# Performance work log

Measured on AMD Instinct MI355X. Metric: run time of the kernel, lower is better.

The kernel has to match this reference:

```python
import jax, jax.numpy as jnp
import numpy as np

N = 100000   # nodes
E = 1600000  # edges (before self-loops)
IN = 128     # in_dim
H = 32       # hidden (hardcoded in module)
G = 2048     # graphs in batch
NEG_SLOPE = 0.2  # PyG GATConv default leaky_relu slope


def setup_inputs() -> dict:
    key = jax.random.key(0)
    ks = jax.random.split(key, 20)
    inp = {
        "x": jax.random.normal(ks[0], (N, IN), jnp.float32),
        "edge_index": jax.random.randint(ks[1], (2, E), 0, N, dtype=jnp.int64),
        "batch": jnp.sort(jax.random.randint(ks[2], (N,), 0, G, dtype=jnp.int64)),
    }
    dims = [(IN, H), (H, H), (H, H), (H, H)]
    for i, (di, do) in enumerate(dims, start=1):
        k = 3 + 4 * (i - 1)
        inp[f"W{i}"] = jax.random.normal(ks[k], (di, do), jnp.float32) * 0.1
        inp[f"a_s{i}"] = jax.random.normal(ks[k + 1], (do,), jnp.float32) * 0.1
        inp[f"a_d{i}"] = jax.random.normal(ks[k + 2], (do,), jnp.float32) * 0.1
        inp[f"b{i}"] = jnp.zeros((do,), jnp.float32)
    return inp


def _gat(x, src, dst, W, a_s, a_d, b):
    # PyG GATConv, heads=1: h = xW; e_ij = leaky_relu(a_s.h_j + a_d.h_i);
    # alpha = softmax over incoming edges of i; out_i = sum_j alpha_ij * h_j + b
    h = x @ W                                # [N, H]
    es = h @ a_s                             # [N]
    ed = h @ a_d                             # [N]
    e = jax.nn.leaky_relu(es[src] + ed[dst], NEG_SLOPE)   # [E+N]
    m = jax.ops.segment_max(e, dst, num_segments=N)        # per-dest max (stable softmax)
    ex = jnp.exp(e - m[dst])
    denom = jax.ops.segment_sum(ex, dst, num_segments=N)
    alpha = ex / denom[dst]
    out = jax.ops.segment_sum(alpha[:, None] * h[src], dst, num_segments=N)
    return out + b


def reference(x, edge_index, batch, W1, a_s1, a_d1, b1, W2, a_s2, a_d2, b2,
              W3, a_s3, a_d3, b3, W4, a_s4, a_d4, b4):
    # add self-loops once (GATConv add_self_loops=True; same edge set every layer)
    loop = jnp.arange(N, dtype=edge_index.dtype)
    src = jnp.concatenate([edge_index[0], loop])
    dst = jnp.concatenate([edge_index[1], loop])
    x = _gat(x, src, dst, W1, a_s1, a_d1, b1)  # tanh in source is a no-op (result discarded)
    x = _gat(x, src, dst, W2, a_s2, a_d2, b2)
    x = _gat(x, src, dst, W3, a_s3, a_d3, b3)
    x = _gat(x, src, dst, W4, a_s4, a_d4, b4)
    # global_mean_pool
    sums = jax.ops.segment_sum(x, batch, num_segments=G)
    cnt = jax.ops.segment_sum(jnp.ones((N,), x.dtype), batch, num_segments=G)
    return sums / jnp.maximum(cnt, 1.0)[:, None]
```

## Files before the change

kernel.cpp:

```cpp
#include <hip/hip_runtime.h>
#include <hip/hip_fp16.h>

#define HDIM 32
#define IN_DIM 128
#define NEG_SLOPE 0.2f
#define NPB 128
#define NPB_SHIFT 7
#define MAXB 1024
#define CHUNK 8192
#define CAP 4096

typedef _Float16 half8  __attribute__((ext_vector_type(8)));
typedef _Float16 half4v __attribute__((ext_vector_type(4)));
typedef float    floatx4 __attribute__((ext_vector_type(4)));

__device__ __forceinline__ float leaky(float e) {
    return (e >= 0.f) ? e : NEG_SLOPE * e;
}

__device__ __forceinline__ float2 h2f(unsigned int u) {
    __half2 h = *reinterpret_cast<__half2*>(&u);
    return __half22float2(h);
}


template<int K>
__global__ __launch_bounds__(256) void gemm_mfma(
    const float* __restrict__ x, const float* __restrict__ W,
    const float* __restrict__ a_s, const float* __restrict__ a_d,
    __half* __restrict__ h, float* __restrict__ es, float* __restrict__ ed, int N)
{
    constexpr int KP = K + 8;
    __shared__ _Float16 xs[64 * KP];
    __shared__ _Float16 Wt[32 * KP];
    const int tid = threadIdx.x;
    for (int i = tid; i < K * 32; i += 256) {
        int k = i >> 5, n = i & 31;
        Wt[n * KP + k] = (_Float16)W[i];
    }
    const int lane = tid & 63;
    const int wave = tid >> 6;
    const int m16  = lane & 15;
    const int quad = lane >> 4;
    const float as0 = a_s[m16], as1 = a_s[m16 + 16];
    const float ad0 = a_d[m16], ad1 = a_d[m16 + 16];

    const int ntiles = (N + 63) >> 6;
    for (int tile = blockIdx.x; tile < ntiles; tile += gridDim.x) {
        const int row0 = tile << 6;
        __syncthreads();
        for (int i = tid; i < 64 * (K / 4); i += 256) {
            int r  = i / (K / 4);
            int c4 = i % (K / 4);
            float4 v = (row0 + r < N) ? ((const float4*)x)[(size_t)(row0 + r) * (K / 4) + c4]
                                      : make_float4(0.f, 0.f, 0.f, 0.f);
            half4v hv = { (_Float16)v.x, (_Float16)v.y, (_Float16)v.z, (_Float16)v.w };
            *(half4v*)&xs[r * KP + c4 * 4] = hv;
        }
        __syncthreads();
        floatx4 acc0 = {0.f, 0.f, 0.f, 0.f}, acc1 = {0.f, 0.f, 0.f, 0.f};
        const int rbase = wave * 16;
        #pragma unroll
        for (int kt = 0; kt < K / 32; kt++) {
            half8 a  = *(half8*)&xs[(rbase + m16) * KP + kt * 32 + quad * 8];
            half8 b0 = *(half8*)&Wt[m16 * KP + kt * 32 + quad * 8];
            half8 b1 = *(half8*)&Wt[(m16 + 16) * KP + kt * 32 + quad * 8];
            acc0 = __builtin_amdgcn_mfma_f32_16x16x32_f16(a, b0, acc0, 0, 0, 0);
            acc1 = __builtin_amdgcn_mfma_f32_16x16x32_f16(a, b1, acc1, 0, 0, 0);
        }
        #pragma unroll
        for (int r = 0; r < 4; r++) {
            int row = row0 + rbase + quad * 4 + r;
            float c0 = acc0[r], c1 = acc1[r];
            float ps = c0 * as0 + c1 * as1;
            float pd = c0 * ad0 + c1 * ad1;
            #pragma unroll
            for (int m = 8; m >= 1; m >>= 1) { ps += __shfl_xor(ps, m); pd += __shfl_xor(pd, m); }
            if (row < N) {
                h[(size_t)row * HDIM + m16]      = __float2half(c0);
                h[(size_t)row * HDIM + m16 + 16] = __float2half(c1);
                if (m16 == 0) { es[row] = ps; ed[row] = pd; }
            }
        }
    }
}


__global__ __launch_bounds__(256) void chunk_hist(
    const int* __restrict__ dsts, int E, int B, int* __restrict__ cnt2D)
{
    __shared__ int hist[MAXB];
    const int blk = blockIdx.x;
    for (int i = threadIdx.x; i < B; i += 256) hist[i] = 0;
    __syncthreads();
    const int e0 = blk * CHUNK;
    for (int i = threadIdx.x; i < CHUNK; i += 256) {
        int e = e0 + i;
        if (e < E) atomicAdd(&hist[dsts[e] >> NPB_SHIFT], 1);
    }
    __syncthreads();
    for (int i = threadIdx.x; i < B; i += 256) cnt2D[(size_t)blk * B + i] = hist[i];
}

__global__ __launch_bounds__(256) void chunk_scan(
    const int* __restrict__ cnt2D, int NBLK, int B,
    int* __restrict__ off2D, int* __restrict__ bcnt)
{
    __shared__ int s[256];
    const int b = blockIdx.x, t = threadIdx.x;
    int v = (t < NBLK) ? cnt2D[(size_t)t * B + b] : 0;
    s[t] = v;
    __syncthreads();
    for (int off = 1; off < 256; off <<= 1) {
        int add = (t >= off) ? s[t - off] : 0;
        __syncthreads();
        s[t] += add;
        __syncthreads();
    }
    if (t < NBLK) off2D[(size_t)t * B + b] = s[t] - v;
    if (t == 255) bcnt[b] = s[255];
}

__global__ __launch_bounds__(1024) void bucket_scan(
    const int* __restrict__ bcnt, int B, int E,
    int* __restrict__ bstart, int* __restrict__ rowptr, int N)
{
    __shared__ int s[1024];
    const int t = threadIdx.x;
    int v = (t < B) ? bcnt[t] : 0;
    s[t] = v;
    __syncthreads();
    for (int off = 1; off < 1024; off <<= 1) {
        int add = (t >= off) ? s[t - off] : 0;
        __syncthreads();
        s[t] += add;
        __syncthreads();
    }
    if (t < B) bstart[t] = s[t] - v;
    if (t == 0) { bstart[B] = E; rowptr[N] = E; }
}

__global__ __launch_bounds__(256) void pair_scatter2(
    const int* __restrict__ srcs, const int* __restrict__ dsts, int E, int B,
    const int* __restrict__ off2D, const int* __restrict__ bstart,
    int* __restrict__ pairs)
{
    __shared__ int cur[MAXB];
    const int blk = blockIdx.x;
    for (int i = threadIdx.x; i < B; i += 256)
        cur[i] = bstart[i] + off2D[(size_t)blk * B + i];
    __syncthreads();
    const int e0 = blk * CHUNK;
    for (int i = threadIdx.x; i < CHUNK; i += 256) {
        int e = e0 + i;
        if (e < E) {
            int s = srcs[e], d = dsts[e];
            int pos = atomicAdd(&cur[d >> NPB_SHIFT], 1);
            pairs[pos] = (s << NPB_SHIFT) | (d & (NPB - 1));
        }
    }
}

__global__ __launch_bounds__(256) void bucket_sort(
    const int* __restrict__ pairs, const int* __restrict__ bstart,
    int* __restrict__ rowptr, int* __restrict__ csrsrc, int N)
{
    __shared__ int ldeg[NPB];
    __shared__ int lex[NPB];
    __shared__ int recs[CAP];
    __shared__ int sorted[CAP];
    const int b = blockIdx.x, t = threadIdx.x;
    const int p0 = bstart[b], p1 = bstart[b + 1];
    const int cnt = p1 - p0;
    if (t < NPB) ldeg[t] = 0;
    __syncthreads();
    for (int i = t; i < cnt; i += 256) {
        int r = pairs[p0 + i];
        atomicAdd(&ldeg[r & (NPB - 1)], 1);
        if (i < CAP) recs[i] = r;
    }
    __syncthreads();
    if (t < NPB) lex[t] = ldeg[t];
    __syncthreads();
    for (int off = 1; off < NPB; off <<= 1) {
        int add = (t >= off && t < NPB) ? lex[t - off] : 0;
        __syncthreads();
        if (t < NPB) lex[t] += add;
        __syncthreads();
    }
    const int node0 = b * NPB;
    if (t < NPB) {
        int excl = lex[t] - ldeg[t];
        if (node0 + t < N) rowptr[node0 + t] = p0 + excl;
        ldeg[t] = excl;
    }
    __syncthreads();
    if (cnt <= CAP) {
        for (int i = t; i < cnt; i += 256) {
            int r = recs[i];
            int pos = atomicAdd(&ldeg[r & (NPB - 1)], 1);
            sorted[pos] = r >> NPB_SHIFT;
        }
        __syncthreads();
        for (int i = t; i < cnt; i += 256) csrsrc[p0 + i] = sorted[i];
    } else {
        for (int i = t; i < cnt; i += 256) {
            int r = pairs[p0 + i];
            int pos = atomicAdd(&ldeg[r & (NPB - 1)], 1);
            csrsrc[p0 + pos] = r >> NPB_SHIFT;
        }
    }
}


__global__ __launch_bounds__(256) void agg5(
    const __half* __restrict__ h, const float* __restrict__ es, const float* __restrict__ ed,
    const int* __restrict__ rowptr, const int* __restrict__ csrsrc,
    const float* __restrict__ a_s, const float* __restrict__ b,
    float* __restrict__ out, int N)
{
    const int gid  = blockIdx.x * 256 + threadIdx.x;
    const int node = gid >> 2;
    const int l    = threadIdx.x & 3;
    if (node >= N) return;

    const int e0 = rowptr[node];
    const int e1 = rowptr[node + 1];
    const float edi = ed[node];
    const uint4* __restrict__ h16 = (const uint4*)h;

    float asf[8];
    #pragma unroll
    for (int i = 0; i < 8; i++) asf[i] = a_s[l * 8 + i];

    float a0=0.f,a1=0.f,a2=0.f,a3=0.f,a4=0.f,a5=0.f,a6=0.f,a7=0.f,den=0.f;

    int e = e0;
    for (; e + 8 <= e1; e += 8) {
        int s[8]; uint4 u[8];
        #pragma unroll
        for (int j = 0; j < 8; j++) s[j] = csrsrc[e + j];
        #pragma unroll
        for (int j = 0; j < 8; j++) u[j] = h16[(size_t)s[j] * 4 + l];
        #pragma unroll
        for (int j = 0; j < 8; j++) {
            float2 f0 = h2f(u[j].x), f1 = h2f(u[j].y), f2 = h2f(u[j].z), f3 = h2f(u[j].w);
            float dot = asf[0]*f0.x + asf[1]*f0.y + asf[2]*f1.x + asf[3]*f1.y
                      + asf[4]*f2.x + asf[5]*f2.y + asf[6]*f3.x + asf[7]*f3.y;
            dot += __shfl_xor(dot, 1);
            dot += __shfl_xor(dot, 2);
            float w = __expf(leaky(dot + edi));
            den += w;
            a0 += w*f0.x; a1 += w*f0.y; a2 += w*f1.x; a3 += w*f1.y;
            a4 += w*f2.x; a5 += w*f2.y; a6 += w*f3.x; a7 += w*f3.y;
        }
    }
    for (; e < e1; e++) {
        int s = csrsrc[e];
        uint4 u = h16[(size_t)s * 4 + l];
        float2 f0 = h2f(u.x), f1 = h2f(u.y), f2 = h2f(u.z), f3 = h2f(u.w);
        float dot = asf[0]*f0.x + asf[1]*f0.y + asf[2]*f1.x + asf[3]*f1.y
                  + asf[4]*f2.x + asf[5]*f2.y + asf[6]*f3.x + asf[7]*f3.y;
        dot += __shfl_xor(dot, 1);
        dot += __shfl_xor(dot, 2);
        float w = __expf(leaky(dot + edi));
        den += w;
        a0 += w*f0.x; a1 += w*f0.y; a2 += w*f1.x; a3 += w*f1.y;
        a4 += w*f2.x; a5 += w*f2.y; a6 += w*f3.x; a7 += w*f3.y;
    }
    {
        float wt = __expf(leaky(es[node] + edi));
        uint4 u = h16[(size_t)node * 4 + l];
        float2 f0 = h2f(u.x), f1 = h2f(u.y), f2 = h2f(u.z), f3 = h2f(u.w);
        den += wt;
        a0 += wt*f0.x; a1 += wt*f0.y; a2 += wt*f1.x; a3 += wt*f1.y;
        a4 += wt*f2.x; a5 += wt*f2.y; a6 += wt*f3.x; a7 += wt*f3.y;
    }
    const float4* b4 = (const float4*)b;
    float4 bv0 = b4[2*l], bv1 = b4[2*l + 1];
    float inv = 1.f / den;
    float4 o0, o1;
    o0.x = a0*inv + bv0.x; o0.y = a1*inv + bv0.y; o0.z = a2*inv + bv0.z; o0.w = a3*inv + bv0.w;
    o1.x = a4*inv + bv1.x; o1.y = a5*inv + bv1.y; o1.z = a6*inv + bv1.z; o1.w = a7*inv + bv1.w;
    ((float4*)out)[(size_t)node*8 + 2*l]     = o0;
    ((float4*)out)[(size_t)node*8 + 2*l + 1] = o1;
}


__global__ __launch_bounds__(256) void pool_graph(
    const float* __restrict__ x, const int* __restrict__ batch,
    float* __restrict__ out, int N, int G)
{
    const int g = (blockIdx.x * 256 + threadIdx.x) >> 6;
    if (g >= G) return;
    const int lane = threadIdx.x & 63;
    const int feat = lane & 31;
    const int half = lane >> 5;

    int lo = 0, hi = N;
    while (lo < hi) { int mid = (lo + hi) >> 1; if (batch[mid] < g) lo = mid + 1; else hi = mid; }
    const int start = lo;
    int lo2 = start, hi2 = N;
    while (lo2 < hi2) { int mid = (lo2 + hi2) >> 1; if (batch[mid] < g + 1) lo2 = mid + 1; else hi2 = mid; }
    const int end = lo2;

    float acc = 0.f;
    for (int i = start + half; i < end; i += 2)
        acc += x[(size_t)i * HDIM + feat];
    acc += __shfl_xor(acc, 32);
    if (half == 0) {
        float cnt = (float)(end - start);
        out[(size_t)g * HDIM + feat] = acc / fmaxf(cnt, 1.f);
    }
}


extern "C" void kernel_launch(void* const* d_in, const int* in_sizes, int n_in,
                              void* d_out, int out_size, void* d_ws, size_t ws_size,
                              hipStream_t stream) {
    const float* x          = (const float*)d_in[0];
    const int*   edge_index = (const int*)d_in[1];
    const int*   batch      = (const int*)d_in[2];

    const int N = in_sizes[2];
    const int E = in_sizes[1] / 2;
    const int G = out_size / HDIM;
    const int B = (N + NPB - 1) / NPB;
    const int NBLK = (E + CHUNK - 1) / CHUNK;
    const int ntiles = (N + 63) / 64;

    const int* srcs = edge_index;
    const int* dsts = edge_index + E;

    char* p = (char*)d_ws;
    __half* h     = (__half*)p; p += (size_t)N * HDIM * sizeof(__half);
    float* xbuf   = (float*)p; p += (size_t)N * HDIM * sizeof(float);
    float* es     = (float*)p; p += (size_t)N * sizeof(float);
    float* ed     = (float*)p; p += (size_t)N * sizeof(float);
    int*   rowptr = (int*)p;   p += (size_t)(N + 1) * sizeof(int);
    int*   csrsrc = (int*)p;   p += (size_t)E * sizeof(int);
    int*   pairs  = (int*)p;   p += (size_t)E * sizeof(int);
    int*   cnt2D  = (int*)p;   p += (size_t)NBLK * B * sizeof(int);
    int*   off2D  = (int*)p;   p += (size_t)NBLK * B * sizeof(int);
    int*   bcnt   = (int*)p;   p += (size_t)B * sizeof(int);
    int*   bstart = (int*)p;   p += (size_t)(B + 1) * sizeof(int);

    chunk_hist  <<<NBLK, 256, 0, stream>>>(dsts, E, B, cnt2D);
    chunk_scan  <<<B, 256, 0, stream>>>(cnt2D, NBLK, B, off2D, bcnt);
    bucket_scan <<<1, 1024, 0, stream>>>(bcnt, B, E, bstart, rowptr, N);
    pair_scatter2<<<NBLK, 256, 0, stream>>>(srcs, dsts, E, B, off2D, bstart, pairs);
    bucket_sort <<<B, 256, 0, stream>>>(pairs, bstart, rowptr, csrsrc, N);

    for (int l = 0; l < 4; l++) {
        const float* W   = (const float*)d_in[3 + 4 * l];
        const float* a_s = (const float*)d_in[4 + 4 * l];
        const float* a_d = (const float*)d_in[5 + 4 * l];
        const float* bb  = (const float*)d_in[6 + 4 * l];

        if (l == 0) gemm_mfma<IN_DIM><<<ntiles, 256, 0, stream>>>(x, W, a_s, a_d, h, es, ed, N);
        else        gemm_mfma<HDIM>  <<<ntiles, 256, 0, stream>>>(xbuf, W, a_s, a_d, h, es, ed, N);

        agg5<<<(N * 4 + 255) / 256, 256, 0, stream>>>(h, es, ed, rowptr, csrsrc, a_s, bb, xbuf, N);
    }

    pool_graph<<<(G * 64 + 255) / 256, 256, 0, stream>>>(xbuf, batch, (float*)d_out, N, G);
}
```

Measured before the change: 346.5 us.

## Fuse next-layer 32x32 projection into aggregation and compute attention scores on the fly

The aggregation kernel now multiplies each node's output by the next layer's 32x32 weight matrix held in shared memory and writes fp16 h directly. This removes three separate gemm launches and the fp32 xbuf round trip between layers. The per-node es/ed scores are no longer produced by the gemm; they are recomputed from the node's own h row inside aggregation. This adds per-thread register pressure (a 32-float row plus a 32-step FMA loop) and an LDS weight load per block, which may reduce occupancy of the gather-bound kernel.

```diff
diff --git a/kernel.cpp b/kernel.cpp
--- a/kernel.cpp
+++ b/kernel.cpp
@@ -27,8 +27,7 @@
 template<int K>
 __global__ __launch_bounds__(256) void gemm_mfma(
     const float* __restrict__ x, const float* __restrict__ W,
-    const float* __restrict__ a_s, const float* __restrict__ a_d,
-    __half* __restrict__ h, float* __restrict__ es, float* __restrict__ ed, int N)
+    __half* __restrict__ h, int N)
 {
     constexpr int KP = K + 8;
     __shared__ _Float16 xs[64 * KP];
@@ -42,8 +41,6 @@
     const int wave = tid >> 6;
     const int m16  = lane & 15;
     const int quad = lane >> 4;
-    const float as0 = a_s[m16], as1 = a_s[m16 + 16];
-    const float ad0 = a_d[m16], ad1 = a_d[m16 + 16];
 
     const int ntiles = (N + 63) >> 6;
     for (int tile = blockIdx.x; tile < ntiles; tile += gridDim.x) {
@@ -71,15 +68,9 @@
         #pragma unroll
         for (int r = 0; r < 4; r++) {
             int row = row0 + rbase + quad * 4 + r;
-            float c0 = acc0[r], c1 = acc1[r];
-            float ps = c0 * as0 + c1 * as1;
-            float pd = c0 * ad0 + c1 * ad1;
-            #pragma unroll
-            for (int m = 8; m >= 1; m >>= 1) { ps += __shfl_xor(ps, m); pd += __shfl_xor(pd, m); }
             if (row < N) {
-                h[(size_t)row * HDIM + m16]      = __float2half(c0);
-                h[(size_t)row * HDIM + m16 + 16] = __float2half(c1);
-                if (m16 == 0) { es[row] = ps; ed[row] = pd; }
+                h[(size_t)row * HDIM + m16]      = __float2half(acc0[r]);
+                h[(size_t)row * HDIM + m16 + 16] = __float2half(acc1[r]);
             }
         }
     }
@@ -213,12 +204,20 @@
 }
 
 
-__global__ __launch_bounds__(256) void agg5(
-    const __half* __restrict__ h, const float* __restrict__ es, const float* __restrict__ ed,
+template<bool LAST>
+__global__ __launch_bounds__(256) void agg_fused(
+    const __half* __restrict__ h,
     const int* __restrict__ rowptr, const int* __restrict__ csrsrc,
-    const float* __restrict__ a_s, const float* __restrict__ b,
-    float* __restrict__ out, int N)
-{
+    const float* __restrict__ a_s, const float* __restrict__ a_d,
+    const float* __restrict__ b, const float* __restrict__ Wn,
+    __half* __restrict__ hn, float* __restrict__ outbuf, int N)
+{
+    __shared__ float Ws[HDIM * HDIM];
+    if (!LAST) {
+        for (int i = threadIdx.x; i < HDIM * HDIM; i += 256) Ws[i] = Wn[i];
+        __syncthreads();
+    }
+
     const int gid  = blockIdx.x * 256 + threadIdx.x;
     const int node = gid >> 2;
     const int l    = threadIdx.x & 3;
@@ -226,12 +225,21 @@
 
     const int e0 = rowptr[node];
     const int e1 = rowptr[node + 1];
-    const float edi = ed[node];
     const uint4* __restrict__ h16 = (const uint4*)h;
 
-    float asf[8];
+    float asf[8], adf[8];
     #pragma unroll
-    for (int i = 0; i < 8; i++) asf[i] = a_s[l * 8 + i];
+    for (int i = 0; i < 8; i++) { asf[i] = a_s[l * 8 + i]; adf[i] = a_d[l * 8 + i]; }
+
+    uint4 uself = h16[(size_t)node * 4 + l];
+    float2 g0 = h2f(uself.x), g1 = h2f(uself.y), g2 = h2f(uself.z), g3 = h2f(uself.w);
+    float dsl = asf[0]*g0.x + asf[1]*g0.y + asf[2]*g1.x + asf[3]*g1.y
+              + asf[4]*g2.x + asf[5]*g2.y + asf[6]*g3.x + asf[7]*g3.y;
+    float ddl = adf[0]*g0.x + adf[1]*g0.y + adf[2]*g1.x + adf[3]*g1.y
+              + adf[4]*g2.x + adf[5]*g2.y + adf[6]*g3.x + adf[7]*g3.y;
+    dsl += __shfl_xor(dsl, 1); dsl += __shfl_xor(dsl, 2);
+    ddl += __shfl_xor(ddl, 1); ddl += __shfl_xor(ddl, 2);
+    const float edi = ddl;
 
     float a0=0.f,a1=0.f,a2=0.f,a3=0.f,a4=0.f,a5=0.f,a6=0.f,a7=0.f,den=0.f;
 
@@ -269,21 +277,44 @@
         a4 += w*f2.x; a5 += w*f2.y; a6 += w*f3.x; a7 += w*f3.y;
     }
     {
-        float wt = __expf(leaky(es[node] + edi));
-        uint4 u = h16[(size_t)node * 4 + l];
-        float2 f0 = h2f(u.x), f1 = h2f(u.y), f2 = h2f(u.z), f3 = h2f(u.w);
-        den += wt;
-        a0 += wt*f0.x; a1 += wt*f0.y; a2 += wt*f1.x; a3 += wt*f1.y;
-        a4 += wt*f2.x; a5 += wt*f2.y; a6 += wt*f3.x; a7 += wt*f3.y;
-    }
+        float w = __expf(leaky(dsl + edi));
+        den += w;
+        a0 += w*g0.x; a1 += w*g0.y; a2 += w*g1.x; a3 += w*g1.y;
+        a4 += w*g2.x; a5 += w*g2.y; a6 += w*g3.x; a7 += w*g3.y;
+    }
+
     const float4* b4 = (const float4*)b;
     float4 bv0 = b4[2*l], bv1 = b4[2*l + 1];
     float inv = 1.f / den;
-    float4 o0, o1;
-    o0.x = a0*inv + bv0.x; o0.y = a1*inv + bv0.y; o0.z = a2*inv + bv0.z; o0.w = a3*inv + bv0.w;
-    o1.x = a4*inv + bv1.x; o1.y = a5*inv + bv1.y; o1.z = a6*inv + bv1.z; o1.w = a7*inv + bv1.w;
-    ((float4*)out)[(size_t)node*8 + 2*l]     = o0;
-    ((float4*)out)[(size_t)node*8 + 2*l + 1] = o1;
+    float o[8];
+    o[0] = a0*inv + bv0.x; o[1] = a1*inv + bv0.y; o[2] = a2*inv + bv0.z; o[3] = a3*inv + bv0.w;
+    o[4] = a4*inv + bv1.x; o[5] = a5*inv + bv1.y; o[6] = a6*inv + bv1.z; o[7] = a7*inv + bv1.w;
+
+    if (LAST) {
+        float4 o0 = { o[0], o[1], o[2], o[3] };
+        float4 o1 = { o[4], o[5], o[6], o[7] };
+        ((float4*)outbuf)[(size_t)node*8 + 2*l]     = o0;
+        ((float4*)outbuf)[(size_t)node*8 + 2*l + 1] = o1;
+    } else {
+        float row[32];
+        #pragma unroll
+        for (int bb = 0; bb < 4; bb++) {
+            #pragma unroll
+            for (int j = 0; j < 8; j++) row[bb*8 + j] = __shfl(o[j], bb, 4);
+        }
+        float hn8[8] = {0.f,0.f,0.f,0.f,0.f,0.f,0.f,0.f};
+        #pragma unroll
+        for (int k = 0; k < 32; k++) {
+            float4 wa = *(const float4*)&Ws[k*32 + l*8];
+            float4 wb = *(const float4*)&Ws[k*32 + l*8 + 4];
+            float rk = row[k];
+            hn8[0] += rk*wa.x; hn8[1] += rk*wa.y; hn8[2] += rk*wa.z; hn8[3] += rk*wa.w;
+            hn8[4] += rk*wb.x; hn8[5] += rk*wb.y; hn8[6] += rk*wb.z; hn8[7] += rk*wb.w;
+        }
+        half8 v = { (_Float16)hn8[0], (_Float16)hn8[1], (_Float16)hn8[2], (_Float16)hn8[3],
+                    (_Float16)hn8[4], (_Float16)hn8[5], (_Float16)hn8[6], (_Float16)hn8[7] };
+        *(half8*)((_Float16*)hn + (size_t)node*32 + l*8) = v;
+    }
 }
 
 
@@ -333,11 +364,11 @@
     const int* dsts = edge_index + E;
 
     char* p = (char*)d_ws;
-    __half* h     = (__half*)p; p += (size_t)N * HDIM * sizeof(__half);
+    __half* h_a   = (__half*)p; p += (size_t)N * HDIM * sizeof(__half);
+    __half* h_b   = (__half*)p; p += (size_t)N * HDIM * sizeof(__half);
     float* xbuf   = (float*)p; p += (size_t)N * HDIM * sizeof(float);
-    float* es     = (float*)p; p += (size_t)N * sizeof(float);
-    float* ed     = (float*)p; p += (size_t)N * sizeof(float);
     int*   rowptr = (int*)p;   p += (size_t)(N + 1) * sizeof(int);
+    p += 16 - ((size_t)p & 15);
     int*   csrsrc = (int*)p;   p += (size_t)E * sizeof(int);
     int*   pairs  = (int*)p;   p += (size_t)E * sizeof(int);
     int*   cnt2D  = (int*)p;   p += (size_t)NBLK * B * sizeof(int);
@@ -351,17 +382,30 @@
     pair_scatter2<<<NBLK, 256, 0, stream>>>(srcs, dsts, E, B, off2D, bstart, pairs);
     bucket_sort <<<B, 256, 0, stream>>>(pairs, bstart, rowptr, csrsrc, N);
 
-    for (int l = 0; l < 4; l++) {
-        const float* W   = (const float*)d_in[3 + 4 * l];
-        const float* a_s = (const float*)d_in[4 + 4 * l];
-        const float* a_d = (const float*)d_in[5 + 4 * l];
-        const float* bb  = (const float*)d_in[6 + 4 * l];
-
-        if (l == 0) gemm_mfma<IN_DIM><<<ntiles, 256, 0, stream>>>(x, W, a_s, a_d, h, es, ed, N);
-        else        gemm_mfma<HDIM>  <<<ntiles, 256, 0, stream>>>(xbuf, W, a_s, a_d, h, es, ed, N);
-
-        agg5<<<(N * 4 + 255) / 256, 256, 0, stream>>>(h, es, ed, rowptr, csrsrc, a_s, bb, xbuf, N);
-    }
+    const float* W1   = (const float*)d_in[3];
+    const float* as1  = (const float*)d_in[4];
+    const float* ad1  = (const float*)d_in[5];
+    const float* b1   = (const float*)d_in[6];
+    const float* W2   = (const float*)d_in[7];
+    const float* as2  = (const float*)d_in[8];
+    const float* ad2  = (const float*)d_in[9];
+    const float* b2   = (const float*)d_in[10];
+    const float* W3   = (const float*)d_in[11];
+    const float* as3  = (const float*)d_in[12];
+    const float* ad3  = (const float*)d_in[13];
+    const float* b3   = (const float*)d_in[14];
+    const float* W4   = (const float*)d_in[15];
+    const float* as4  = (const float*)d_in[16];
+    const float* ad4  = (const float*)d_in[17];
+    const float* b4   = (const float*)d_in[18];
+
+    const int aggGrid = (N * 4 + 255) / 256;
+
+    gemm_mfma<IN_DIM><<<ntiles, 256, 0, stream>>>(x, W1, h_a, N);
+    agg_fused<false><<<aggGrid, 256, 0, stream>>>(h_a, rowptr, csrsrc, as1, ad1, b1, W2, h_b, xbuf, N);
+    agg_fused<false><<<aggGrid, 256, 0, stream>>>(h_b, rowptr, csrsrc, as2, ad2, b2, W3, h_a, xbuf, N);
+    agg_fused<false><<<aggGrid, 256, 0, stream>>>(h_a, rowptr, csrsrc, as3, ad3, b3, W4, h_b, xbuf, N);
+    agg_fused<true> <<<aggGrid, 256, 0, stream>>>(h_b, rowptr, csrsrc, as4, ad4, b4, W4, h_a, xbuf, N);
 
     pool_graph<<<(G * 64 + 255) / 256, 256, 0, stream>>>(xbuf, batch, (float*)d_out, N, G);
 }
```

Result: slower. 363.8 us (+5.0%).

## Sort nodes by degree for aggregation and compute self attention scores in-kernel

Applied to the files above, without the earlier changes.

Adds a degree-bucketed permutation of destination nodes (histogram, scan and scatter kernels run once), so that aggregation waves process nodes with similar in-degree and suffer less divergence. It also removes the es/ed outputs from the GEMM epilogue and recomputes the self node's source and destination scores inside the aggregation kernel from the self row it already loads. The cost is three extra setup kernels, an indirect perm lookup, and output writes scattered across nodes instead of sequential, which can hurt coalescing and locality.

```diff
diff --git a/kernel.cpp b/kernel.cpp
--- a/kernel.cpp
+++ b/kernel.cpp
@@ -9,6 +9,7 @@
 #define MAXB 1024
 #define CHUNK 8192
 #define CAP 4096
+#define DBINS 128
 
 typedef _Float16 half8  __attribute__((ext_vector_type(8)));
 typedef _Float16 half4v __attribute__((ext_vector_type(4)));
@@ -27,8 +28,7 @@
 template<int K>
 __global__ __launch_bounds__(256) void gemm_mfma(
     const float* __restrict__ x, const float* __restrict__ W,
-    const float* __restrict__ a_s, const float* __restrict__ a_d,
-    __half* __restrict__ h, float* __restrict__ es, float* __restrict__ ed, int N)
+    __half* __restrict__ h, int N)
 {
     constexpr int KP = K + 8;
     __shared__ _Float16 xs[64 * KP];
@@ -42,8 +42,6 @@
     const int wave = tid >> 6;
     const int m16  = lane & 15;
     const int quad = lane >> 4;
-    const float as0 = a_s[m16], as1 = a_s[m16 + 16];
-    const float ad0 = a_d[m16], ad1 = a_d[m16 + 16];
 
     const int ntiles = (N + 63) >> 6;
     for (int tile = blockIdx.x; tile < ntiles; tile += gridDim.x) {
@@ -71,15 +69,9 @@
         #pragma unroll
         for (int r = 0; r < 4; r++) {
             int row = row0 + rbase + quad * 4 + r;
-            float c0 = acc0[r], c1 = acc1[r];
-            float ps = c0 * as0 + c1 * as1;
-            float pd = c0 * ad0 + c1 * ad1;
-            #pragma unroll
-            for (int m = 8; m >= 1; m >>= 1) { ps += __shfl_xor(ps, m); pd += __shfl_xor(pd, m); }
             if (row < N) {
-                h[(size_t)row * HDIM + m16]      = __float2half(c0);
-                h[(size_t)row * HDIM + m16 + 16] = __float2half(c1);
-                if (m16 == 0) { es[row] = ps; ed[row] = pd; }
+                h[(size_t)row * HDIM + m16]      = __float2half(acc0[r]);
+                h[(size_t)row * HDIM + m16 + 16] = __float2half(acc1[r]);
             }
         }
     }
@@ -213,25 +205,78 @@
 }
 
 
-__global__ __launch_bounds__(256) void agg5(
-    const __half* __restrict__ h, const float* __restrict__ es, const float* __restrict__ ed,
+__global__ __launch_bounds__(256) void deg_hist(
+    const int* __restrict__ rowptr, int N, int* __restrict__ dhist)
+{
+    int i = blockIdx.x * 256 + threadIdx.x;
+    if (i < N) {
+        int d = rowptr[i + 1] - rowptr[i];
+        if (d > DBINS - 1) d = DBINS - 1;
+        atomicAdd(&dhist[d], 1);
+    }
+}
+
+__global__ __launch_bounds__(DBINS) void deg_scan(
+    const int* __restrict__ dhist, int* __restrict__ dcur)
+{
+    __shared__ int s[DBINS];
+    int t = threadIdx.x;
+    int v = dhist[t];
+    s[t] = v;
+    __syncthreads();
+    for (int off = 1; off < DBINS; off <<= 1) {
+        int add = (t >= off) ? s[t - off] : 0;
+        __syncthreads();
+        s[t] += add;
+        __syncthreads();
+    }
+    dcur[t] = s[t] - v;
+}
+
+__global__ __launch_bounds__(256) void deg_scatter(
+    const int* __restrict__ rowptr, int N,
+    int* __restrict__ dcur, int* __restrict__ perm)
+{
+    int i = blockIdx.x * 256 + threadIdx.x;
+    if (i < N) {
+        int d = rowptr[i + 1] - rowptr[i];
+        if (d > DBINS - 1) d = DBINS - 1;
+        int pos = atomicAdd(&dcur[d], 1);
+        perm[pos] = i;
+    }
+}
+
+
+__global__ __launch_bounds__(256) void agg6(
+    const __half* __restrict__ h,
     const int* __restrict__ rowptr, const int* __restrict__ csrsrc,
-    const float* __restrict__ a_s, const float* __restrict__ b,
-    float* __restrict__ out, int N)
-{
-    const int gid  = blockIdx.x * 256 + threadIdx.x;
-    const int node = gid >> 2;
-    const int l    = threadIdx.x & 3;
-    if (node >= N) return;
+    const int* __restrict__ perm,
+    const float* __restrict__ a_s, const float* __restrict__ a_d,
+    const float* __restrict__ b, float* __restrict__ out, int N)
+{
+    const int gid = blockIdx.x * 256 + threadIdx.x;
+    const int gi  = gid >> 2;
+    const int l   = threadIdx.x & 3;
+    if (gi >= N) return;
+    const int node = perm[gi];
 
     const int e0 = rowptr[node];
     const int e1 = rowptr[node + 1];
-    const float edi = ed[node];
     const uint4* __restrict__ h16 = (const uint4*)h;
 
-    float asf[8];
+    float asf[8], adf[8];
     #pragma unroll
-    for (int i = 0; i < 8; i++) asf[i] = a_s[l * 8 + i];
+    for (int i = 0; i < 8; i++) { asf[i] = a_s[l * 8 + i]; adf[i] = a_d[l * 8 + i]; }
+
+    uint4 uself = h16[(size_t)node * 4 + l];
+    float2 g0 = h2f(uself.x), g1 = h2f(uself.y), g2 = h2f(uself.z), g3 = h2f(uself.w);
+    float dsl = asf[0]*g0.x + asf[1]*g0.y + asf[2]*g1.x + asf[3]*g1.y
+              + asf[4]*g2.x + asf[5]*g2.y + asf[6]*g3.x + asf[7]*g3.y;
+    float ddl = adf[0]*g0.x + adf[1]*g0.y + adf[2]*g1.x + adf[3]*g1.y
+              + adf[4]*g2.x + adf[5]*g2.y + adf[6]*g3.x + adf[7]*g3.y;
+    dsl += __shfl_xor(dsl, 1); dsl += __shfl_xor(dsl, 2);
+    ddl += __shfl_xor(ddl, 1); ddl += __shfl_xor(ddl, 2);
+    const float edi = ddl;
 
     float a0=0.f,a1=0.f,a2=0.f,a3=0.f,a4=0.f,a5=0.f,a6=0.f,a7=0.f,den=0.f;
 
@@ -269,13 +314,12 @@
         a4 += w*f2.x; a5 += w*f2.y; a6 += w*f3.x; a7 += w*f3.y;
     }
     {
-        float wt = __expf(leaky(es[node] + edi));
-        uint4 u = h16[(size_t)node * 4 + l];
-        float2 f0 = h2f(u.x), f1 = h2f(u.y), f2 = h2f(u.z), f3 = h2f(u.w);
-        den += wt;
-        a0 += wt*f0.x; a1 += wt*f0.y; a2 += wt*f1.x; a3 += wt*f1.y;
-        a4 += wt*f2.x; a5 += wt*f2.y; a6 += wt*f3.x; a7 += wt*f3.y;
-    }
+        float w = __expf(leaky(dsl + edi));
+        den += w;
+        a0 += w*g0.x; a1 += w*g0.y; a2 += w*g1.x; a3 += w*g1.y;
+        a4 += w*g2.x; a5 += w*g2.y; a6 += w*g3.x; a7 += w*g3.y;
+    }
+
     const float4* b4 = (const float4*)b;
     float4 bv0 = b4[2*l], bv1 = b4[2*l + 1];
     float inv = 1.f / den;
@@ -335,21 +379,29 @@
     char* p = (char*)d_ws;
     __half* h     = (__half*)p; p += (size_t)N * HDIM * sizeof(__half);
     float* xbuf   = (float*)p; p += (size_t)N * HDIM * sizeof(float);
-    float* es     = (float*)p; p += (size_t)N * sizeof(float);
-    float* ed     = (float*)p; p += (size_t)N * sizeof(float);
     int*   rowptr = (int*)p;   p += (size_t)(N + 1) * sizeof(int);
+    p += 16 - ((size_t)p & 15);
     int*   csrsrc = (int*)p;   p += (size_t)E * sizeof(int);
     int*   pairs  = (int*)p;   p += (size_t)E * sizeof(int);
+    int*   perm   = (int*)p;   p += (size_t)N * sizeof(int);
     int*   cnt2D  = (int*)p;   p += (size_t)NBLK * B * sizeof(int);
     int*   off2D  = (int*)p;   p += (size_t)NBLK * B * sizeof(int);
     int*   bcnt   = (int*)p;   p += (size_t)B * sizeof(int);
     int*   bstart = (int*)p;   p += (size_t)(B + 1) * sizeof(int);
+    int*   dhist  = (int*)p;   p += (size_t)DBINS * sizeof(int);
+    int*   dcur   = (int*)p;   p += (size_t)DBINS * sizeof(int);
 
     chunk_hist  <<<NBLK, 256, 0, stream>>>(dsts, E, B, cnt2D);
     chunk_scan  <<<B, 256, 0, stream>>>(cnt2D, NBLK, B, off2D, bcnt);
     bucket_scan <<<1, 1024, 0, stream>>>(bcnt, B, E, bstart, rowptr, N);
     pair_scatter2<<<NBLK, 256, 0, stream>>>(srcs, dsts, E, B, off2D, bstart, pairs);
     bucket_sort <<<B, 256, 0, stream>>>(pairs, bstart, rowptr, csrsrc, N);
+    hipMemsetAsync(dhist, 0, DBINS * sizeof(int), stream);
+    deg_hist    <<<(N + 255) / 256, 256, 0, stream>>>(rowptr, N, dhist);
+    deg_scan    <<<1, DBINS, 0, stream>>>(dhist, dcur);
+    deg_scatter <<<(N + 255) / 256, 256, 0, stream>>>(rowptr, N, dcur, perm);
+
+    const int aggGrid = (N * 4 + 255) / 256;
 
     for (int l = 0; l < 4; l++) {
         const float* W   = (const float*)d_in[3 + 4 * l];
@@ -357,10 +409,10 @@
         const float* a_d = (const float*)d_in[5 + 4 * l];
         const float* bb  = (const float*)d_in[6 + 4 * l];
 
-        if (l == 0) gemm_mfma<IN_DIM><<<ntiles, 256, 0, stream>>>(x, W, a_s, a_d, h, es, ed, N);
-        else        gemm_mfma<HDIM>  <<<ntiles, 256, 0, stream>>>(xbuf, W, a_s, a_d, h, es, ed, N);
-
-        agg5<<<(N * 4 + 255) / 256, 256, 0, stream>>>(h, es, ed, rowptr, csrsrc, a_s, bb, xbuf, N);
+        if (l == 0) gemm_mfma<IN_DIM><<<ntiles, 256, 0, stream>>>(x, W, h, N);
+        else        gemm_mfma<HDIM>  <<<ntiles, 256, 0, stream>>>(xbuf, W, h, N);
+
+        agg6<<<aggGrid, 256, 0, stream>>>(h, rowptr, csrsrc, perm, a_s, a_d, bb, xbuf, N);
     }
 
     pool_graph<<<(G * 64 + 255) / 256, 256, 0, stream>>>(xbuf, batch, (float*)d_out, N, G);
```

Result: slower. 819.9 us (+136.6%).

## Store hidden features as FP8 and read precomputed source scores in aggregation

Applied to the files above, without the earlier changes.

The GEMM epilogue now stages results in shared memory and packs each row's 32 features into FP8 (32 bytes per row instead of 64 in fp16). The aggregation kernel gathers these FP8 rows and reads the precomputed per-node es value instead of recomputing the a_s dot product and shuffle-reducing it per edge. The aim is to halve the random-gather traffic and cut per-edge arithmetic in the bandwidth-bound aggregation. FP8 storage adds quantization error that compounds across four layers and may exceed tolerance. The GEMM epilogue also gains a block barrier.

```diff
diff --git a/kernel.cpp b/kernel.cpp
--- a/kernel.cpp
+++ b/kernel.cpp
@@ -13,14 +13,10 @@
 typedef _Float16 half8  __attribute__((ext_vector_type(8)));
 typedef _Float16 half4v __attribute__((ext_vector_type(4)));
 typedef float    floatx4 __attribute__((ext_vector_type(4)));
+typedef float    floatx2 __attribute__((ext_vector_type(2)));
 
 __device__ __forceinline__ float leaky(float e) {
     return (e >= 0.f) ? e : NEG_SLOPE * e;
-}
-
-__device__ __forceinline__ float2 h2f(unsigned int u) {
-    __half2 h = *reinterpret_cast<__half2*>(&u);
-    return __half22float2(h);
 }
 
 
@@ -28,11 +24,12 @@
 __global__ __launch_bounds__(256) void gemm_mfma(
     const float* __restrict__ x, const float* __restrict__ W,
     const float* __restrict__ a_s, const float* __restrict__ a_d,
-    __half* __restrict__ h, float* __restrict__ es, float* __restrict__ ed, int N)
+    uint2* __restrict__ h8, float* __restrict__ es, float* __restrict__ ed, int N)
 {
     constexpr int KP = K + 8;
     __shared__ _Float16 xs[64 * KP];
     __shared__ _Float16 Wt[32 * KP];
+    __shared__ float stage[64 * 33];
     const int tid = threadIdx.x;
     for (int i = tid; i < K * 32; i += 256) {
         int k = i >> 5, n = i & 31;
@@ -70,16 +67,29 @@
         }
         #pragma unroll
         for (int r = 0; r < 4; r++) {
-            int row = row0 + rbase + quad * 4 + r;
+            const int lr = rbase + quad * 4 + r;
+            int row = row0 + lr;
             float c0 = acc0[r], c1 = acc1[r];
+            stage[lr * 33 + m16]      = c0;
+            stage[lr * 33 + m16 + 16] = c1;
             float ps = c0 * as0 + c1 * as1;
             float pd = c0 * ad0 + c1 * ad1;
             #pragma unroll
             for (int m = 8; m >= 1; m >>= 1) { ps += __shfl_xor(ps, m); pd += __shfl_xor(pd, m); }
+            if (row < N && m16 == 0) { es[row] = ps; ed[row] = pd; }
+        }
+        __syncthreads();
+        {
+            int r = tid >> 2, seg = tid & 3;
+            int row = row0 + r;
             if (row < N) {
-                h[(size_t)row * HDIM + m16]      = __float2half(c0);
-                h[(size_t)row * HDIM + m16 + 16] = __float2half(c1);
-                if (m16 == 0) { es[row] = ps; ed[row] = pd; }
+                const float* sp = &stage[r * 33 + seg * 8];
+                unsigned int u0, u1;
+                u0 = __builtin_amdgcn_cvt_pk_fp8_f32(sp[0], sp[1], 0,  false);
+                u0 = __builtin_amdgcn_cvt_pk_fp8_f32(sp[2], sp[3], u0, true);
+                u1 = __builtin_amdgcn_cvt_pk_fp8_f32(sp[4], sp[5], 0,  false);
+                u1 = __builtin_amdgcn_cvt_pk_fp8_f32(sp[6], sp[7], u1, true);
+                h8[(size_t)row * 4 + seg] = make_uint2(u0, u1);
             }
         }
     }
@@ -213,11 +223,10 @@
 }
 
 
-__global__ __launch_bounds__(256) void agg5(
-    const __half* __restrict__ h, const float* __restrict__ es, const float* __restrict__ ed,
+__global__ __launch_bounds__(256) void agg7(
+    const uint2* __restrict__ h8, const float* __restrict__ es, const float* __restrict__ ed,
     const int* __restrict__ rowptr, const int* __restrict__ csrsrc,
-    const float* __restrict__ a_s, const float* __restrict__ b,
-    float* __restrict__ out, int N)
+    const float* __restrict__ b, float* __restrict__ out, int N)
 {
     const int gid  = blockIdx.x * 256 + threadIdx.x;
     const int node = gid >> 2;
@@ -227,29 +236,25 @@
     const int e0 = rowptr[node];
     const int e1 = rowptr[node + 1];
     const float edi = ed[node];
-    const uint4* __restrict__ h16 = (const uint4*)h;
-
-    float asf[8];
-    #pragma unroll
-    for (int i = 0; i < 8; i++) asf[i] = a_s[l * 8 + i];
 
     float a0=0.f,a1=0.f,a2=0.f,a3=0.f,a4=0.f,a5=0.f,a6=0.f,a7=0.f,den=0.f;
 
     int e = e0;
     for (; e + 8 <= e1; e += 8) {
-        int s[8]; uint4 u[8];
+        int s[8]; float q[8]; uint2 u[8];
         #pragma unroll
         for (int j = 0; j < 8; j++) s[j] = csrsrc[e + j];
         #pragma unroll
-        for (int j = 0; j < 8; j++) u[j] = h16[(size_t)s[j] * 4 + l];
+        for (int j = 0; j < 8; j++) q[j] = es[s[j]];
+        #pragma unroll
+        for (int j = 0; j < 8; j++) u[j] = h8[(size_t)s[j] * 4 + l];
         #pragma unroll
         for (int j = 0; j < 8; j++) {
-            float2 f0 = h2f(u[j].x), f1 = h2f(u[j].y), f2 = h2f(u[j].z), f3 = h2f(u[j].w);
-            float dot = asf[0]*f0.x + asf[1]*f0.y + asf[2]*f1.x + asf[3]*f1.y
-                      + asf[4]*f2.x + asf[5]*f2.y + asf[6]*f3.x + asf[7]*f3.y;
-            dot += __shfl_xor(dot, 1);
-            dot += __shfl_xor(dot, 2);
-            float w = __expf(leaky(dot + edi));
+            floatx2 f0 = __builtin_amdgcn_cvt_pk_f32_fp8(u[j].x, false);
+            floatx2 f1 = __builtin_amdgcn_cvt_pk_f32_fp8(u[j].x, true);
+            floatx2 f2 = __builtin_amdgcn_cvt_pk_f32_fp8(u[j].y, false);
+            floatx2 f3 = __builtin_amdgcn_cvt_pk_f32_fp8(u[j].y, true);
+            float w = __expf(leaky(q[j] + edi));
             den += w;
             a0 += w*f0.x; a1 += w*f0.y; a2 += w*f1.x; a3 += w*f1.y;
             a4 += w*f2.x; a5 += w*f2.y; a6 += w*f3.x; a7 += w*f3.y;
@@ -257,25 +262,29 @@
     }
     for (; e < e1; e++) {
         int s = csrsrc[e];
-        uint4 u = h16[(size_t)s * 4 + l];
-        float2 f0 = h2f(u.x), f1 = h2f(u.y), f2 = h2f(u.z), f3 = h2f(u.w);
-        float dot = asf[0]*f0.x + asf[1]*f0.y + asf[2]*f1.x + asf[3]*f1.y
-                  + asf[4]*f2.x + asf[5]*f2.y + asf[6]*f3.x + asf[7]*f3.y;
-        dot += __shfl_xor(dot, 1);
-        dot += __shfl_xor(dot, 2);
-        float w = __expf(leaky(dot + edi));
+        float q = es[s];
+        uint2 u = h8[(size_t)s * 4 + l];
+        floatx2 f0 = __builtin_amdgcn_cvt_pk_f32_fp8(u.x, false);
+        floatx2 f1 = __builtin_amdgcn_cvt_pk_f32_fp8(u.x, true);
+        floatx2 f2 = __builtin_amdgcn_cvt_pk_f32_fp8(u.y, false);
+        floatx2 f3 = __builtin_amdgcn_cvt_pk_f32_fp8(u.y, true);
+        float w = __expf(leaky(q + edi));
         den += w;
         a0 += w*f0.x; a1 += w*f0.y; a2 += w*f1.x; a3 += w*f1.y;
         a4 += w*f2.x; a5 += w*f2.y; a6 += w*f3.x; a7 += w*f3.y;
     }
     {
-        float wt = __expf(leaky(es[node] + edi));
-        uint4 u = h16[(size_t)node * 4 + l];
-        float2 f0 = h2f(u.x), f1 = h2f(u.y), f2 = h2f(u.z), f3 = h2f(u.w);
-        den += wt;
-        a0 += wt*f0.x; a1 += wt*f0.y; a2 += wt*f1.x; a3 += wt*f1.y;
-        a4 += wt*f2.x; a5 += wt*f2.y; a6 += wt*f3.x; a7 += wt*f3.y;
-    }
+        float w = __expf(leaky(es[node] + edi));
+        uint2 u = h8[(size_t)node * 4 + l];
+        floatx2 f0 = __builtin_amdgcn_cvt_pk_f32_fp8(u.x, false);
+        floatx2 f1 = __builtin_amdgcn_cvt_pk_f32_fp8(u.x, true);
+        floatx2 f2 = __builtin_amdgcn_cvt_pk_f32_fp8(u.y, false);
+        floatx2 f3 = __builtin_amdgcn_cvt_pk_f32_fp8(u.y, true);
+        den += w;
+        a0 += w*f0.x; a1 += w*f0.y; a2 += w*f1.x; a3 += w*f1.y;
+        a4 += w*f2.x; a5 += w*f2.y; a6 += w*f3.x; a7 += w*f3.y;
+    }
+
     const float4* b4 = (const float4*)b;
     float4 bv0 = b4[2*l], bv1 = b4[2*l + 1];
     float inv = 1.f / den;
@@ -333,11 +342,12 @@
     const int* dsts = edge_index + E;
 
     char* p = (char*)d_ws;
-    __half* h     = (__half*)p; p += (size_t)N * HDIM * sizeof(__half);
+    uint2* h8     = (uint2*)p; p += (size_t)N * 4 * sizeof(uint2);
     float* xbuf   = (float*)p; p += (size_t)N * HDIM * sizeof(float);
     float* es     = (float*)p; p += (size_t)N * sizeof(float);
     float* ed     = (float*)p; p += (size_t)N * sizeof(float);
     int*   rowptr = (int*)p;   p += (size_t)(N + 1) * sizeof(int);
+    p += 16 - ((size_t)p & 15);
     int*   csrsrc = (int*)p;   p += (size_t)E * sizeof(int);
     int*   pairs  = (int*)p;   p += (size_t)E * sizeof(int);
     int*   cnt2D  = (int*)p;   p += (size_t)NBLK * B * sizeof(int);
@@ -351,16 +361,18 @@
     pair_scatter2<<<NBLK, 256, 0, stream>>>(srcs, dsts, E, B, off2D, bstart, pairs);
     bucket_sort <<<B, 256, 0, stream>>>(pairs, bstart, rowptr, csrsrc, N);
 
+    const int aggGrid = (N * 4 + 255) / 256;
+
     for (int l = 0; l < 4; l++) {
         const float* W   = (const float*)d_in[3 + 4 * l];
         const float* a_s = (const float*)d_in[4 + 4 * l];
         const float* a_d = (const float*)d_in[5 + 4 * l];
         const float* bb  = (const float*)d_in[6 + 4 * l];
 
-        if (l == 0) gemm_mfma<IN_DIM><<<ntiles, 256, 0, stream>>>(x, W, a_s, a_d, h, es, ed, N);
-        else        gemm_mfma<HDIM>  <<<ntiles, 256, 0, stream>>>(xbuf, W, a_s, a_d, h, es, ed, N);
-
-        agg5<<<(N * 4 + 255) / 256, 256, 0, stream>>>(h, es, ed, rowptr, csrsrc, a_s, bb, xbuf, N);
+        if (l == 0) gemm_mfma<IN_DIM><<<ntiles, 256, 0, stream>>>(x, W, a_s, a_d, h8, es, ed, N);
+        else        gemm_mfma<HDIM>  <<<ntiles, 256, 0, stream>>>(xbuf, W, a_s, a_d, h8, es, ed, N);
+
+        agg7<<<aggGrid, 256, 0, stream>>>(h8, es, ed, rowptr, csrsrc, bb, xbuf, N);
     }
 
     pool_graph<<<(G * 64 + 255) / 256, 256, 0, stream>>>(xbuf, batch, (float*)d_out, N, G);
```

Result: faster. 331.0 us (-4.5%).
